# Performance work log

Measured on AMD Instinct MI355X. Metric: run time of the kernel, lower is better.

## Reference

```python
import jax, jax.numpy as jnp
import numpy as np


def _layernorm(x, g, b, eps=1e-5):
    m = x.mean(-1, keepdims=True)
    v = ((x - m) ** 2).mean(-1, keepdims=True)
    return (x - m) / jnp.sqrt(v + eps) * g + b


def _rotate_every_two(x):
    x1 = x[..., ::2]
    x2 = x[..., 1::2]
    return jnp.stack([-x2, x1], axis=-1).reshape(x.shape)


def _segsum(x):
    # x: (..., L) of negative decay rates -> (..., L, L) bidirectional segment sums
    cs = jnp.cumsum(x, axis=-1)
    d = cs[..., :, None] - cs[..., None, :]
    L = x.shape[-1]
    i = jnp.arange(L)[:, None]
    j = jnp.arange(L)[None, :]
    # lower-tri (incl diag): cs[i]-cs[j]; strict upper: cs[j]-cs[i]; diag is 0
    return jnp.where(i >= j, d, -d)


def _forward(x, y, th, dw1_w, dw1_b, dw2_w, dw2_b, qw, qb, kw, kb, vw, vb,
             lepe_w, lepe_b, dt_w, dt_bias, A_log, ow, ob,
             n1_g, n1_b, ffn_w1, ffn_b1, ffn_w2, ffn_b2, n2_g, n2_b):
    B, C, H, W = x.shape
    nh = dt_bias.shape[0]
    hd = C // nh
    scaling = hd ** (-0.5)

    # dynamic gated fusion of the two kv branches (1x1 convs == channel matmuls)
    fusion = jnp.concatenate([y, th], axis=1)                      # (B,2C,H,W)
    hid = jax.nn.relu(jnp.einsum('bchw,oc->bohw', fusion, dw1_w) + dw1_b[None, :, None, None])
    logits = jnp.einsum('bchw,oc->bohw', hid, dw2_w) + dw2_b[None, :, None, None]
    wts = jax.nn.softmax(logits, axis=1)                           # (B,2,H,W)
    fused = y * wts[:, 0:1] + th * wts[:, 1:2]

    xh = jnp.transpose(x, (0, 2, 3, 1))                            # (B,H,W,C)
    fkv = jnp.transpose(fused, (0, 2, 3, 1))

    # 2D RoPE tables (flattened raster index)
    angle = jnp.repeat(1.0 / 10000 ** jnp.linspace(0.0, 1.0, hd // 2), 2)
    idx = jnp.arange(H * W, dtype=x.dtype)
    sin = jnp.sin(idx[:, None] * angle[None, :]).reshape(H, W, hd)
    cos = jnp.cos(idx[:, None] * angle[None, :]).reshape(H, W, hd)

    q = xh @ qw + qb
    k = fkv @ kw + kb
    v = fkv @ vw + vb

    # depthwise 5x5 conv position term on v (NHWC)
    lepe = jax.lax.conv_general_dilated(
        v, lepe_w, (1, 1), ((2, 2), (2, 2)),
        dimension_numbers=('NHWC', 'HWIO', 'NHWC'), feature_group_count=C) + lepe_b

    k = k * scaling
    q = q.reshape(B, H, W, nh, hd).transpose(0, 3, 1, 2, 4)        # (B,nh,H,W,hd)
    k = k.reshape(B, H, W, nh, hd).transpose(0, 3, 1, 2, 4)
    v5 = v.reshape(B, H, W, nh, hd).transpose(0, 3, 1, 2, 4)

    qr = q * cos + _rotate_every_two(q) * sin
    kr = k * cos + _rotate_every_two(k) * sin

    # PathEmbeding2D: data-dependent decay masks
    xt = xh.reshape(B, H * W, nh, hd)
    dt = xt @ dt_w                                                 # (B,S,nh,2)
    A = -jnp.exp(A_log)                                            # (nh,)
    da = jax.nn.softplus(dt[..., 0] + dt_bias) * A                 # (B,S,nh)
    db = jax.nn.softplus(dt[..., 1] + dt_bias) * A
    mask_w = _segsum(da.reshape(B, H, W, nh).transpose(0, 1, 3, 2))  # (B,H,nh,W,W)
    mask_h = _segsum(db.reshape(B, H, W, nh).transpose(0, 2, 3, 1))  # (B,W,nh,H,H)

    # row (width-direction) and column (height-direction) attentions
    qk_w = jax.nn.softmax(jnp.einsum('bnhid,bnhjd->bhnij', qr, kr) + mask_w, axis=-1)  # (B,H,nh,W,W)
    qk_h = jax.nn.softmax(jnp.einsum('bnhwd,bngwd->bwnhg', qr, kr) + mask_h, axis=-1)  # (B,W,nh,H,H)

    v_w = jnp.einsum('bhnij,bnhjd->bhnid', qk_w, v5)               # (B,H,nh,W,hd)
    out1 = jnp.einsum('bwnhg,bgnwd->bwnhd', qk_h, v_w)             # (B,W,nh,H,hd)
    out1 = out1.transpose(0, 3, 1, 2, 4).reshape(B, H, W, C)

    v_h = jnp.einsum('bwnhg,bngwd->bwnhd', qk_h, v5)               # (B,W,nh,H,hd)
    out2 = jnp.einsum('bhnij,bjnhd->bhnid', qk_w, v_h)             # (B,H,nh,W,hd)
    out2 = out2.transpose(0, 1, 3, 2, 4).reshape(B, H, W, C)

    out = 0.5 * out1 + 0.5 * out2 + lepe
    out = out @ ow + ob
    out = _layernorm(xh + out, n1_g, n1_b)
    ffn = jax.nn.gelu(out @ ffn_w1 + ffn_b1, approximate=False) @ ffn_w2 + ffn_b2
    out = _layernorm(out + ffn, n2_g, n2_b)
    return jnp.transpose(out, (0, 3, 1, 2))                        # (B,C,H,W)


def setup_inputs() -> dict:
    B, C, H, W, nh = 4, 64, 128, 128, 4
    hd = C // nh
    key = jax.random.key(0)
    ks = jax.random.split(key, 20)
    n = lambda k, shp, s: jax.random.normal(k, shp, dtype=jnp.float32) * s
    rng = np.random.default_rng(0)
    dt = np.exp(rng.uniform(0.0, 1.0, nh) * (np.log(0.1) - np.log(0.001)) + np.log(0.001))
    dt = np.clip(dt, 1e-4, None)
    dt_bias = jnp.asarray(dt + np.log(-np.expm1(-dt)), dtype=jnp.float32)
    A_log = jnp.asarray(np.log(rng.uniform(1.0, 1.1, nh)), dtype=jnp.float32)
    inp = {
        'x': n(ks[0], (B, C, H, W), 1.0),
        'y': n(ks[1], (B, C, H, W), 1.0),
        'th': n(ks[2], (B, C, H, W), 1.0),
        'dw1_w': n(ks[3], (C, 2 * C), (2 * C) ** -0.5),
        'dw1_b': jnp.zeros((C,), jnp.float32),
        'dw2_w': n(ks[4], (2, C), C ** -0.5),
        'dw2_b': jnp.zeros((2,), jnp.float32),
        'qw': n(ks[5], (C, C), 0.2 * C ** -0.5),
        'qb': jnp.zeros((C,), jnp.float32),
        'kw': n(ks[6], (C, C), 0.2 * C ** -0.5),
        'kb': jnp.zeros((C,), jnp.float32),
        'vw': n(ks[7], (C, C), 0.2 * C ** -0.5),
        'vb': jnp.zeros((C,), jnp.float32),
        'lepe_w': n(ks[8], (5, 5, 1, C), 0.1),
        'lepe_b': jnp.zeros((C,), jnp.float32),
        'dt_w': n(ks[9], (hd, 2), hd ** -0.5),
        'dt_bias': dt_bias,
        'A_log': A_log,
        'ow': n(ks[10], (C, C), C ** -0.5),
        'ob': jnp.zeros((C,), jnp.float32),
        'n1_g': jnp.ones((C,), jnp.float32),
        'n1_b': jnp.zeros((C,), jnp.float32),
        'ffn_w1': n(ks[11], (C, 4 * C), C ** -0.5),
        'ffn_b1': jnp.zeros((4 * C,), jnp.float32),
        'ffn_w2': n(ks[12], (4 * C, C), (4 * C) ** -0.5),
        'ffn_b2': jnp.zeros((C,), jnp.float32),
        'n2_g': jnp.ones((C,), jnp.float32),
        'n2_b': jnp.zeros((C,), jnp.float32),
    }
    return inp


def reference(x, y, th, dw1_w, dw1_b, dw2_w, dw2_b, qw, qb, kw, kb, vw, vb,
              lepe_w, lepe_b, dt_w, dt_bias, A_log, ow, ob,
              n1_g, n1_b, ffn_w1, ffn_b1, ffn_w2, ffn_b2, n2_g, n2_b):
    return _forward(x, y, th, dw1_w, dw1_b, dw2_w, dw2_b, qw, qb, kw, kb, vw, vb,
                    lepe_w, lepe_b, dt_w, dt_bias, A_log, ow, ob,
                    n1_g, n1_b, ffn_w1, ffn_b1, ffn_w2, ffn_b2, n2_g, n2_b)
```

## Files before the change

kernel.cpp:

```cpp
#include <hip/hip_runtime.h>
#include <math.h>

#define HWSZ 16384

typedef __attribute__((ext_vector_type(8))) short bf16x8;
typedef __attribute__((ext_vector_type(4))) float f32x4;
typedef unsigned short u16;

union U4 { uint4 v; u16 s[8]; };
union U2 { uint2 v; u16 s[4]; };

__device__ __forceinline__ float gelu_f(float v) {
    return 0.5f * v * (1.0f + erff(v * 0.70710678118654752f));
}
__device__ __forceinline__ float splus_f(float v) {
    return (v > 20.f) ? v : log1pf(expf(v));
}
__device__ __forceinline__ u16 f2bf(float f) {
    union { float f; unsigned u; } v; v.f = f;
    unsigned r = (v.u + 0x7FFF + ((v.u >> 16) & 1)) >> 16;
    return (u16)r;
}
__device__ __forceinline__ unsigned pk2(float a, float b) {
    return (unsigned)f2bf(a) | ((unsigned)f2bf(b) << 16);
}
__device__ __forceinline__ float bf2f(u16 s) {
    union { unsigned u; float f; } v; v.u = ((unsigned)s) << 16; return v.f;
}

#define FS 136
__global__ __launch_bounds__(256) void k_fuse(
    const float* __restrict__ y, const float* __restrict__ th,
    const float* __restrict__ w1, const float* __restrict__ b1,
    const float* __restrict__ w2, const float* __restrict__ b2,
    u16* __restrict__ fused)
{
    __shared__ u16 Fsh[128*FS];
    __shared__ u16 Wt[64*FS];
    int tid = threadIdx.x, bid = blockIdx.x;
    int pbase = bid*128;
    int b = pbase >> 14, p0 = pbase & 16383;
    for (int vi = tid; vi < 1024; vi += 256) {
        int cp = vi >> 5;
        int p4 = (vi & 31)*4;
        int c0 = cp*2;
        float4 a = *(const float4*)&y [((size_t)(b*64+c0  ))*HWSZ + p0 + p4];
        float4 c = *(const float4*)&y [((size_t)(b*64+c0+1))*HWSZ + p0 + p4];
        *(unsigned*)&Fsh[(p4+0)*FS + c0] = pk2(a.x, c.x);
        *(unsigned*)&Fsh[(p4+1)*FS + c0] = pk2(a.y, c.y);
        *(unsigned*)&Fsh[(p4+2)*FS + c0] = pk2(a.z, c.z);
        *(unsigned*)&Fsh[(p4+3)*FS + c0] = pk2(a.w, c.w);
        float4 e = *(const float4*)&th[((size_t)(b*64+c0  ))*HWSZ + p0 + p4];
        float4 f = *(const float4*)&th[((size_t)(b*64+c0+1))*HWSZ + p0 + p4];
        *(unsigned*)&Fsh[(p4+0)*FS + 64 + c0] = pk2(e.x, f.x);
        *(unsigned*)&Fsh[(p4+1)*FS + 64 + c0] = pk2(e.y, f.y);
        *(unsigned*)&Fsh[(p4+2)*FS + 64 + c0] = pk2(e.z, f.z);
        *(unsigned*)&Fsh[(p4+3)*FS + 64 + c0] = pk2(e.w, f.w);
    }
    for (int vi = tid; vi < 2048; vi += 256) {
        int o = vi >> 5, c4 = (vi & 31)*4;
        float4 wv = *(const float4*)&w1[o*128 + c4];
        *(unsigned*)&Wt[o*FS + c4]     = pk2(wv.x, wv.y);
        *(unsigned*)&Wt[o*FS + c4 + 2] = pk2(wv.z, wv.w);
    }
    __syncthreads();
    int lane = tid & 63, wv = tid >> 6;
    int quad = lane >> 4, lm = lane & 15;
    int M0 = wv*32;
    f32x4 z = {0.f,0.f,0.f,0.f};
    f32x4 acc[2][4];
    #pragma unroll
    for (int mt = 0; mt < 2; ++mt)
        #pragma unroll
        for (int nt = 0; nt < 4; ++nt) acc[mt][nt] = z;
    #pragma unroll
    for (int ks = 0; ks < 4; ++ks) {
        bf16x8 aF[2];
        #pragma unroll
        for (int mt = 0; mt < 2; ++mt)
            aF[mt] = *(bf16x8*)&Fsh[(M0+mt*16+lm)*FS + ks*32 + quad*8];
        #pragma unroll
        for (int nt = 0; nt < 4; ++nt) {
            bf16x8 bW = *(bf16x8*)&Wt[(nt*16+lm)*FS + ks*32 + quad*8];
            #pragma unroll
            for (int mt = 0; mt < 2; ++mt)
                acc[mt][nt] = __builtin_amdgcn_mfma_f32_16x16x32_bf16(aF[mt], bW, acc[mt][nt], 0,0,0);
        }
    }
    float b1v[4], w2av[4], w2bv[4];
    #pragma unroll
    for (int nt = 0; nt < 4; ++nt) {
        int o = nt*16 + lm;
        b1v[nt] = b1[o]; w2av[nt] = w2[o]; w2bv[nt] = w2[64+o];
    }
    float bias2a = b2[0], bias2b = b2[1];
    size_t gbase = (size_t)(b*16384 + p0);
// ... 2 lines not shown
        #pragma unroll
        for (int r = 0; r < 4; ++r) {
            int p = M0 + mt*16 + quad*4 + r;
            float l0 = 0.f, l1 = 0.f;
            #pragma unroll
            for (int nt = 0; nt < 4; ++nt) {
                float h = fmaxf(acc[mt][nt][r] + b1v[nt], 0.f);
                l0 += h * w2av[nt];
                l1 += h * w2bv[nt];
            }
            l0 += __shfl_xor(l0,1,64); l0 += __shfl_xor(l0,2,64);
            l0 += __shfl_xor(l0,4,64); l0 += __shfl_xor(l0,8,64);
            l1 += __shfl_xor(l1,1,64); l1 += __shfl_xor(l1,2,64);
            l1 += __shfl_xor(l1,4,64); l1 += __shfl_xor(l1,8,64);
            l0 += bias2a; l1 += bias2b;
            float m = fmaxf(l0, l1);
            float e0 = __expf(l0 - m), e1 = __expf(l1 - m);
            float inv = 1.f/(e0 + e1);
            float wa = e0*inv, wb = e1*inv;
            U2 yv, tv;
            yv.v = *(uint2*)&Fsh[p*FS + lm*4];
            tv.v = *(uint2*)&Fsh[p*FS + 64 + lm*4];
            unsigned o0 = pk2(bf2f(yv.s[0])*wa + bf2f(tv.s[0])*wb,
                              bf2f(yv.s[1])*wa + bf2f(tv.s[1])*wb);
            unsigned o1 = pk2(bf2f(yv.s[2])*wa + bf2f(tv.s[2])*wb,
                              bf2f(yv.s[3])*wa + bf2f(tv.s[3])*wb);
            *(uint2*)&fused[(gbase + p)*64 + lm*4] = make_uint2(o0, o1);
        }
    }
}

__global__ __launch_bounds__(256) void k_qkv(
    const float* __restrict__ x, const u16* __restrict__ fused,
    const float* __restrict__ qw, const float* __restrict__ qb,
    const float* __restrict__ kw, const float* __restrict__ kb,
    const float* __restrict__ vw, const float* __restrict__ vb,
    const float* __restrict__ dtw, const float* __restrict__ dtb,
    const float* __restrict__ alog,
    u16* __restrict__ qr, u16* __restrict__ kr, u16* __restrict__ v5,
    float* __restrict__ da, float* __restrict__ db)
{
    __shared__ u16 Ax[128*72];
    __shared__ u16 Af[128*72];
    __shared__ u16 Bq[64*72], Bk[64*72], Bv[64*72];
    int tid = threadIdx.x, bid = blockIdx.x;
    int pbase = bid*128;
    int b = pbase >> 14, p0 = pbase & 16383;
    for (int vi = tid; vi < 2048; vi += 256) {
        int c = vi >> 5, pg = (vi & 31)*4;
        float4 xv = *(const float4*)&x[((size_t)(b*64+c))*HWSZ + p0 + pg];
        Ax[(pg+0)*72 + c] = f2bf(xv.x);
        Ax[(pg+1)*72 + c] = f2bf(xv.y);
        Ax[(pg+2)*72 + c] = f2bf(xv.z);
        Ax[(pg+3)*72 + c] = f2bf(xv.w);
    }
    for (int vi = tid; vi < 1024; vi += 256) {
        int p = vi >> 3, seg = (vi & 7)*8;
        *(uint4*)&Af[p*72 + seg] = *(const uint4*)&fused[((size_t)(b*16384) + p0 + p)*64 + seg];
    }
    for (int vi = tid; vi < 1024; vi += 256) {
        int c = vi >> 4, o4 = (vi & 15)*4;
        float4 q = *(const float4*)&qw[c*64 + o4];
        float4 k = *(const float4*)&kw[c*64 + o4];
        float4 v = *(const float4*)&vw[c*64 + o4];
        Bq[(o4+0)*72+c]=f2bf(q.x); Bq[(o4+1)*72+c]=f2bf(q.y); Bq[(o4+2)*72+c]=f2bf(q.z); Bq[(o4+3)*72+c]=f2bf(q.w);
        Bk[(o4+0)*72+c]=f2bf(k.x); Bk[(o4+1)*72+c]=f2bf(k.y); Bk[(o4+2)*72+c]=f2bf(k.z); Bk[(o4+3)*72+c]=f2bf(k.w);
        Bv[(o4+0)*72+c]=f2bf(v.x); Bv[(o4+1)*72+c]=f2bf(v.y); Bv[(o4+2)*72+c]=f2bf(v.z); Bv[(o4+3)*72+c]=f2bf(v.w);
    }
    __syncthreads();
    int lane = tid & 63, wv = tid >> 6;
    int quad = lane >> 4, lm = lane & 15;
    int M0 = wv*32;
    f32x4 z = {0.f,0.f,0.f,0.f};
    f32x4 accQ[2][4], accK[2][4], accV[2][4];
    #pragma unroll
    for (int mt = 0; mt < 2; ++mt)
        #pragma unroll
        for (int nt = 0; nt < 4; ++nt) { accQ[mt][nt]=z; accK[mt][nt]=z; accV[mt][nt]=z; }
    #pragma unroll
    for (int ks = 0; ks < 2; ++ks) {
        bf16x8 aX[2], aF[2];
        #pragma unroll
        for (int mt = 0; mt < 2; ++mt) {
            aX[mt] = *(bf16x8*)&Ax[(M0+mt*16+lm)*72 + ks*32 + quad*8];
            aF[mt] = *(bf16x8*)&Af[(M0+mt*16+lm)*72 + ks*32 + quad*8];
        }
        #pragma unroll
        for (int nt = 0; nt < 4; ++nt) {
            bf16x8 bQ = *(bf16x8*)&Bq[(nt*16+lm)*72 + ks*32 + quad*8];
            bf16x8 bK = *(bf16x8*)&Bk[(nt*16+lm)*72 + ks*32 + quad*8];
            bf16x8 bV = *(bf16x8*)&Bv[(nt*16+lm)*72 + ks*32 + quad*8];
            #pragma unroll
            for (int mt = 0; mt < 2; ++mt) {
                accQ[mt][nt] = __builtin_amdgcn_mfma_f32_16x16x32_bf16(aX[mt], bQ, accQ[mt][nt], 0,0,0);
                accK[mt][nt] = __builtin_amdgcn_mfma_f32_16x16x32_bf16(aF[mt], bK, accK[mt][nt], 0,0,0);
                accV[mt][nt] = __builtin_amdgcn_mfma_f32_16x16x32_bf16(aF[mt], bV, accV[mt][nt], 0,0,0);
            }
        }
    }
    {
        float dtw_[32];
        #pragma unroll
        for (int i = 0; i < 32; ++i) dtw_[i] = dtw[i];
        #pragma unroll
        for (int rep = 0; rep < 2; ++rep) {
            int pair = tid + rep*256;
            int p = pair >> 2, n = pair & 3;
            float dt0 = 0.f, dt1 = 0.f;
            #pragma unroll
            for (int d = 0; d < 16; ++d) {
                float xv = bf2f(Ax[p*72 + n*16 + d]);
                dt0 += xv*dtw_[2*d];
                dt1 += xv*dtw_[2*d+1];
            }
            float A = -expf(alog[n]);
            float bb = dtb[n];
            int P = p0 + p;
            int h = P >> 7, w = P & 127;
            da[((b*128+h)*4+n)*128 + w] = splus_f(dt0+bb)*A;
            db[((b*128+w)*4+n)*128 + h] = splus_f(dt1+bb)*A;
        }
    }
    float qbv[4], kbv[4], vbv[4];
    #pragma unroll
    for (int nt = 0; nt < 4; ++nt) {
        qbv[nt] = qb[nt*16+lm]; kbv[nt] = kb[nt*16+lm]; vbv[nt] = vb[nt*16+lm];
    }
    bool evn = !(lm & 1);
    float ang = exp2f(-1.89824462565f * (float)(lm >> 1));
    int bb4 = b*4;
    #pragma unroll
    for (int mt = 0; mt < 2; ++mt) {
        #pragma unroll
        for (int r = 0; r < 4; ++r) {
            int P = p0 + M0 + mt*16 + quad*4 + r;
            float sn_, cs_;
            sincosf((float)P * ang, &sn_, &cs_);
            #pragma unroll
            for (int nt = 0; nt < 4; ++nt) {
                float vq = accQ[mt][nt][r] + qbv[nt];
                float pq = __shfl_xor(vq, 1, 64);
                float rq = evn ? vq*cs_ - pq*sn_ : vq*cs_ + pq*sn_;
                unsigned uq = f2bf(rq);
                unsigned upq = (unsigned)__shfl_xor((int)uq, 1, 64);
                float vk = (accK[mt][nt][r] + kbv[nt])*0.25f;
                float pk = __shfl_xor(vk, 1, 64);
                float rk = evn ? vk*cs_ - pk*sn_ : vk*cs_ + pk*sn_;
                unsigned uk = f2bf(rk);
                unsigned upk = (unsigned)__shfl_xor((int)uk, 1, 64);
                unsigned uv = f2bf(accV[mt][nt][r] + vbv[nt]);
                unsigned upv = (unsigned)__shfl_xor((int)uv, 1, 64);
                if (evn) {
                    size_t off = ((size_t)(bb4+nt)*HWSZ + P)*16 + lm;
                    *(unsigned*)&qr[off] = (uq & 0xffff) | (upq << 16);
                    *(unsigned*)&kr[off] = (uk & 0xffff) | (upk << 16);
                    *(unsigned*)&v5[off] = (uv & 0xffff) | (upv << 16);
                }
            }
        }
    }
}

#define LROW 328
__global__ __launch_bounds__(256) void k_lepe(
    const u16* __restrict__ v5, const float* __restrict__ lw,
    const float* __restrict__ lb, u16* __restrict__ lepe)
{
    __shared__ float sv[36*LROW];
    __shared__ float swt[400];
    int tid = threadIdx.x, bid = blockIdx.x;
    int tw = bid & 7, th_ = (bid >> 3) & 3, n = (bid >> 5) & 3, b = bid >> 7;
    int bn = b*4 + n;
    int h0 = th_*32, w0 = tw*16;
    for (int i = tid; i < 400; i += 256) {
        int tap = i >> 4, d = i & 15;
        swt[i] = lw[tap*64 + n*16 + d];
    }
    const u16* vb = v5 + (size_t)bn*HWSZ*16;
// ... 349 lines not shown
    #pragma unroll
    for (int c = 0; c < 4; ++c) {
        bf16x8 bV  = *(bf16x8*)&Vt[lm*136 + c*32 + quad*8];
        bf16x8 aP0 = *(bf16x8*)&Ps[(r0+lm)*136 + c*32 + quad*8];
        bf16x8 aP1 = *(bf16x8*)&Ps[(r1+lm)*136 + c*32 + quad*8];
        acc0 = __builtin_amdgcn_mfma_f32_16x16x32_bf16(aP0, bV, acc0, 0,0,0);
        acc1 = __builtin_amdgcn_mfma_f32_16x16x32_bf16(aP1, bV, acc1, 0,0,0);
    }
    size_t lpb = (size_t)bn*262144 + (size_t)h*2048;
    size_t oab = (size_t)b*1048576 + (size_t)h*8192 + n*16;
    bool evn = !(lm & 1);
    #pragma unroll
    for (int r = 0; r < 4; ++r) {
        int i0 = r0+quad*4+r, i1 = r1+quad*4+r;
        float o2a = acc0[r]*linv[i0];
        float o2b = acc1[r]*linv[i1];
        float o1a = bf2f(o1b[vbase + (size_t)i0*2048 + lm]);
        float o1c = bf2f(o1b[vbase + (size_t)i1*2048 + lm]);
        float la  = bf2f(lepe[lpb + (size_t)i0*16 + lm]);
        float lc  = bf2f(lepe[lpb + (size_t)i1*16 + lm]);
        unsigned ua = f2bf(0.5f*(o1a + o2a) + la);
        unsigned uc = f2bf(0.5f*(o1c + o2b) + lc);
        unsigned upa = (unsigned)__shfl_xor((int)ua,1,64);
        unsigned upc = (unsigned)__shfl_xor((int)uc,1,64);
        if (evn) {
            *(unsigned*)&attn[oab + (size_t)i0*64 + lm] = (ua & 0xffff) | (upa << 16);
            *(unsigned*)&attn[oab + (size_t)i1*64 + lm] = (uc & 0xffff) | (upc << 16);
        }
    }
}

__global__ __launch_bounds__(256) void k_proj_ln(
    const u16* __restrict__ attn, const float* __restrict__ x,
    const float* __restrict__ ow, const float* __restrict__ ob,
    const float* __restrict__ g1, const float* __restrict__ b1,
    u16* __restrict__ t1)
{
    __shared__ u16 As[128*72];
    __shared__ u16 Bs[64*72];
    __shared__ float XT[8704];
    int tid = threadIdx.x, bid = blockIdx.x;
    int pbase = bid*128;
    int b = pbase >> 14, p0 = pbase & 16383;
    for (int vi = tid; vi < 1024; vi += 256) {
        int p = vi >> 3, seg = (vi & 7)*8;
        *(uint4*)&As[p*72 + seg] = *(const uint4*)&attn[((size_t)(pbase+p))*64 + seg];
    }
    for (int vi = tid; vi < 512; vi += 256) {
        int kp = vi >> 4, c4 = (vi & 15)*4;
        float4 a = *(const float4*)&ow[(2*kp)*64 + c4];
        float4 c = *(const float4*)&ow[(2*kp+1)*64 + c4];
        *(unsigned*)&Bs[(c4+0)*72 + 2*kp] = pk2(a.x, c.x);
        *(unsigned*)&Bs[(c4+1)*72 + 2*kp] = pk2(a.y, c.y);
        *(unsigned*)&Bs[(c4+2)*72 + 2*kp] = pk2(a.z, c.z);
        *(unsigned*)&Bs[(c4+3)*72 + 2*kp] = pk2(a.w, c.w);
    }
    for (int vi = tid; vi < 2048; vi += 256) {
        int c = vi >> 5, p4 = (vi & 31)*4;
        *(float4*)&XT[c*132 + p4] = *(const float4*)&x[((size_t)(b*64+c))*HWSZ + p0 + p4];
    }
    __syncthreads();
    int lane = tid & 63, wv = tid >> 6;
    int quad = lane >> 4, lm = lane & 15;
    int M0 = wv*32;
    float xv[2][4][4], obv[4], g1v[4], b1v[4];
    #pragma unroll
    for (int nt = 0; nt < 4; ++nt) {
        int c = nt*16 + lm;
        obv[nt] = ob[c]; g1v[nt] = g1[c]; b1v[nt] = b1[c];
        #pragma unroll
        for (int mt = 0; mt < 2; ++mt)
            #pragma unroll
            for (int r = 0; r < 4; ++r)
                xv[mt][nt][r] = XT[c*132 + M0 + mt*16 + quad*4 + r];
    }
    f32x4 z = {0.f,0.f,0.f,0.f};
    f32x4 acc[2][4];
    #pragma unroll
    for (int mt = 0; mt < 2; ++mt)
        #pragma unroll
        for (int nt = 0; nt < 4; ++nt) acc[mt][nt] = z;
    #pragma unroll
    for (int ks = 0; ks < 2; ++ks) {
        bf16x8 aF[2];
        #pragma unroll
        for (int mt = 0; mt < 2; ++mt)
            aF[mt] = *(bf16x8*)&As[(M0+mt*16+lm)*72 + ks*32 + quad*8];
        #pragma unroll
        for (int nt = 0; nt < 4; ++nt) {
            bf16x8 bF = *(bf16x8*)&Bs[(nt*16+lm)*72 + ks*32 + quad*8];
            #pragma unroll
            for (int mt = 0; mt < 2; ++mt)
                acc[mt][nt] = __builtin_amdgcn_mfma_f32_16x16x32_bf16(aF[mt], bF, acc[mt][nt], 0,0,0);
        }
    }
    float val[2][4][4], res[2][4][4];
    #pragma unroll
    for (int mt = 0; mt < 2; ++mt) {
        #pragma unroll
        for (int r = 0; r < 4; ++r) {
            float s = 0.f;
            #pragma unroll
            for (int nt = 0; nt < 4; ++nt) {
                val[mt][nt][r] = acc[mt][nt][r] + obv[nt] + xv[mt][nt][r];
                s += val[mt][nt][r];
            }
            s += __shfl_xor(s, 1, 64); s += __shfl_xor(s, 2, 64);
            s += __shfl_xor(s, 4, 64); s += __shfl_xor(s, 8, 64);
            float mean = s*(1.f/64.f);
            float vv = 0.f;
            #pragma unroll
            for (int nt = 0; nt < 4; ++nt) {
                float d = val[mt][nt][r] - mean;
                vv += d*d;
            }
            vv += __shfl_xor(vv, 1, 64); vv += __shfl_xor(vv, 2, 64);
            vv += __shfl_xor(vv, 4, 64); vv += __shfl_xor(vv, 8, 64);
            float rs = rsqrtf(vv*(1.f/64.f) + 1e-5f);
            #pragma unroll
            for (int nt = 0; nt < 4; ++nt)
                res[mt][nt][r] = (val[mt][nt][r] - mean)*rs*g1v[nt] + b1v[nt];
        }
    }
    __syncthreads();
    float* outT = XT;
    #pragma unroll
    for (int mt = 0; mt < 2; ++mt)
        #pragma unroll
        for (int r = 0; r < 4; ++r)
            #pragma unroll
            for (int nt = 0; nt < 4; ++nt)
                outT[(M0+mt*16+quad*4+r)*68 + nt*16 + lm] = res[mt][nt][r];
    __syncthreads();
    for (int vi = tid; vi < 1024; vi += 256) {
        int p = vi >> 3, seg = (vi & 7)*8;
        float4 f0 = *(const float4*)&outT[p*68 + seg];
        float4 f1 = *(const float4*)&outT[p*68 + seg + 4];
        uint4 o = make_uint4(pk2(f0.x,f0.y), pk2(f0.z,f0.w), pk2(f1.x,f1.y), pk2(f1.z,f1.w));
        *(uint4*)&t1[((size_t)(pbase+p))*64 + seg] = o;
    }
}

__global__ __launch_bounds__(256) void k_ffn(
    const u16* __restrict__ t1, const float* __restrict__ w1,
    const float* __restrict__ b1f, const float* __restrict__ w2,
    const float* __restrict__ b2f, const float* __restrict__ g2,
    const float* __restrict__ bb2, float* __restrict__ outp)
{
    __shared__ u16 At1[128*72];
    __shared__ u16 WH[2*64*72 + 128*72];
    __shared__ float sb1[256];
    __shared__ float sb2[64], sg[64], sbb[64];
    u16* W1b = WH;
    u16* W2b = WH + 4608;
    u16* Hid = WH + 9216;
    int tid = threadIdx.x, bid = blockIdx.x;
    int pbase = bid*128;
    int b = pbase >> 14, p0 = pbase & 16383;
    for (int vi = tid; vi < 1024; vi += 256) {
        int p = vi >> 3, seg = (vi & 7)*8;
        *(uint4*)&At1[p*72 + seg] = *(const uint4*)&t1[((size_t)(pbase+p))*64 + seg];
    }
    if (tid < 256) sb1[tid] = b1f[tid];
    if (tid < 64) { sb2[tid] = b2f[tid]; sg[tid] = g2[tid]; sbb[tid] = bb2[tid]; }
    int lane = tid & 63, wv = tid >> 6;
    int quad = lane >> 4, lm = lane & 15;
    int M0 = wv*32;
    f32x4 z = {0.f,0.f,0.f,0.f};
    f32x4 acc2[2][4];
    #pragma unroll
    for (int mt = 0; mt < 2; ++mt)
        #pragma unroll
        for (int nt = 0; nt < 4; ++nt) acc2[mt][nt] = z;
    for (int jc = 0; jc < 4; ++jc) {
        __syncthreads();
        for (int vi = tid; vi < 512; vi += 256) {
            int kp = vi >> 4, c4 = (vi & 15)*4;
            float4 a = *(const float4*)&w1[(2*kp)*256 + jc*64 + c4];
            float4 c = *(const float4*)&w1[(2*kp+1)*256 + jc*64 + c4];
            *(unsigned*)&W1b[(c4+0)*72 + 2*kp] = pk2(a.x, c.x);
            *(unsigned*)&W1b[(c4+1)*72 + 2*kp] = pk2(a.y, c.y);
            *(unsigned*)&W1b[(c4+2)*72 + 2*kp] = pk2(a.z, c.z);
            *(unsigned*)&W1b[(c4+3)*72 + 2*kp] = pk2(a.w, c.w);
        }
        for (int vi = tid; vi < 512; vi += 256) {
            int kp = vi >> 4, c4 = (vi & 15)*4;
            float4 a = *(const float4*)&w2[(size_t)(jc*64 + 2*kp)*64 + c4];
            float4 c = *(const float4*)&w2[(size_t)(jc*64 + 2*kp+1)*64 + c4];
            *(unsigned*)&W2b[(c4+0)*72 + 2*kp] = pk2(a.x, c.x);
            *(unsigned*)&W2b[(c4+1)*72 + 2*kp] = pk2(a.y, c.y);
            *(unsigned*)&W2b[(c4+2)*72 + 2*kp] = pk2(a.z, c.z);
            *(unsigned*)&W2b[(c4+3)*72 + 2*kp] = pk2(a.w, c.w);
        }
        __syncthreads();
        f32x4 h[2][4];
        #pragma unroll
        for (int mt = 0; mt < 2; ++mt)
            #pragma unroll
            for (int nt = 0; nt < 4; ++nt) h[mt][nt] = z;
        #pragma unroll
        for (int ks = 0; ks < 2; ++ks) {
            bf16x8 aF[2];
            #pragma unroll
            for (int mt = 0; mt < 2; ++mt)
                aF[mt] = *(bf16x8*)&At1[(M0+mt*16+lm)*72 + ks*32 + quad*8];
            #pragma unroll
            for (int nt = 0; nt < 4; ++nt) {
                bf16x8 bF = *(bf16x8*)&W1b[(nt*16+lm)*72 + ks*32 + quad*8];
                #pragma unroll
                for (int mt = 0; mt < 2; ++mt)
                    h[mt][nt] = __builtin_amdgcn_mfma_f32_16x16x32_bf16(aF[mt], bF, h[mt][nt], 0,0,0);
            }
        }
        #pragma unroll
        for (int nt = 0; nt < 4; ++nt) {
            float bb = sb1[jc*64 + nt*16 + lm];
            #pragma unroll
            for (int mt = 0; mt < 2; ++mt)
                #pragma unroll
                for (int r = 0; r < 4; ++r) {
                    float hv = gelu_f(h[mt][nt][r] + bb);
                    unsigned u = (unsigned)f2bf(hv);
                    unsigned up = (unsigned)__shfl_xor((int)u, 1, 64);
                    if (!(lm & 1))
                        *(unsigned*)&Hid[(M0+mt*16+quad*4+r)*72 + nt*16 + lm] = (u & 0xffff) | (up << 16);
                }
        }
        #pragma unroll
        for (int ks = 0; ks < 2; ++ks) {
            bf16x8 aH[2];
            #pragma unroll
            for (int mt = 0; mt < 2; ++mt)
                aH[mt] = *(bf16x8*)&Hid[(M0+mt*16+lm)*72 + ks*32 + quad*8];
            #pragma unroll
            for (int nt = 0; nt < 4; ++nt) {
                bf16x8 bF = *(bf16x8*)&W2b[(nt*16+lm)*72 + ks*32 + quad*8];
                #pragma unroll
                for (int mt = 0; mt < 2; ++mt)
                    acc2[mt][nt] = __builtin_amdgcn_mfma_f32_16x16x32_bf16(aH[mt], bF, acc2[mt][nt], 0,0,0);
            }
        }
    }
    float val[2][4][4], res[2][4][4];
    float sb2v[4], sgv[4], sbbv[4];
    #pragma unroll
    for (int nt = 0; nt < 4; ++nt) {
        int c = nt*16 + lm;
        sb2v[nt] = sb2[c]; sgv[nt] = sg[c]; sbbv[nt] = sbb[c];
    }
    #pragma unroll
    for (int mt = 0; mt < 2; ++mt) {
        #pragma unroll
        for (int r = 0; r < 4; ++r) {
            int pos = M0 + mt*16 + quad*4 + r;
            float s = 0.f;
            #pragma unroll
            for (int nt = 0; nt < 4; ++nt) {
                float tv = bf2f(At1[pos*72 + nt*16 + lm]);
                val[mt][nt][r] = acc2[mt][nt][r] + sb2v[nt] + tv;
                s += val[mt][nt][r];
            }
            s += __shfl_xor(s, 1, 64); s += __shfl_xor(s, 2, 64);
            s += __shfl_xor(s, 4, 64); s += __shfl_xor(s, 8, 64);
            float mean = s*(1.f/64.f);
            float vv = 0.f;
            #pragma unroll
            for (int nt = 0; nt < 4; ++nt) {
                float d = val[mt][nt][r] - mean;
                vv += d*d;
            }
            vv += __shfl_xor(vv, 1, 64); vv += __shfl_xor(vv, 2, 64);
            vv += __shfl_xor(vv, 4, 64); vv += __shfl_xor(vv, 8, 64);
            float rs = rsqrtf(vv*(1.f/64.f) + 1e-5f);
            #pragma unroll
            for (int nt = 0; nt < 4; ++nt)
                res[mt][nt][r] = (val[mt][nt][r] - mean)*rs*sgv[nt] + sbbv[nt];
        }
    }
    __syncthreads();
    float* outT = (float*)WH;
    #pragma unroll
    for (int mt = 0; mt < 2; ++mt)
        #pragma unroll
        for (int r = 0; r < 4; ++r)
            #pragma unroll
            for (int nt = 0; nt < 4; ++nt)
                outT[(nt*16+lm)*132 + M0 + mt*16 + quad*4 + r] = res[mt][nt][r];
    __syncthreads();
    for (int vi = tid; vi < 2048; vi += 256) {
        int c = vi >> 5, p4 = (vi & 31)*4;
        *(float4*)&outp[((size_t)(b*64+c))*HWSZ + p0 + p4] = *(const float4*)&outT[c*132 + p4];
    }
}

extern "C" void kernel_launch(void* const* d_in, const int* in_sizes, int n_in,
                              void* d_out, int out_size, void* d_ws, size_t ws_size,
                              hipStream_t stream) {
    const float* x      = (const float*)d_in[0];
    const float* y      = (const float*)d_in[1];
    const float* th     = (const float*)d_in[2];
    const float* dw1_w  = (const float*)d_in[3];
    const float* dw1_b  = (const float*)d_in[4];
    const float* dw2_w  = (const float*)d_in[5];
    const float* dw2_b  = (const float*)d_in[6];
    const float* qw     = (const float*)d_in[7];
    const float* qb     = (const float*)d_in[8];
    const float* kw     = (const float*)d_in[9];
    const float* kb     = (const float*)d_in[10];
    const float* vw     = (const float*)d_in[11];
    const float* vb     = (const float*)d_in[12];
    const float* lepe_w = (const float*)d_in[13];
    const float* lepe_b = (const float*)d_in[14];
    const float* dt_w   = (const float*)d_in[15];
    const float* dt_bias= (const float*)d_in[16];
    const float* A_log  = (const float*)d_in[17];
    const float* ow     = (const float*)d_in[18];
    const float* ob     = (const float*)d_in[19];
    const float* n1_g   = (const float*)d_in[20];
    const float* n1_b   = (const float*)d_in[21];
    const float* ffn_w1 = (const float*)d_in[22];
    const float* ffn_b1 = (const float*)d_in[23];
    const float* ffn_w2 = (const float*)d_in[24];
    const float* ffn_b2 = (const float*)d_in[25];
    const float* n2_g   = (const float*)d_in[26];
    const float* n2_b   = (const float*)d_in[27];
    float* out = (float*)d_out;

    const size_t SZ = 4194304;
    float* ws    = (float*)d_ws;
    u16* fused = (u16*)(ws + 0*SZ);
    u16* qrb   = (u16*)(ws + 1*SZ);
    u16* krb   = (u16*)(ws + 2*SZ);
    u16* v5b   = (u16*)(ws + 3*SZ);
    u16* lepeb = (u16*)(ws + 4*SZ);
    u16* vhb   = (u16*)(ws + 5*SZ);
    u16* o1b   = (u16*)(ws + 6*SZ);
    u16* attnb = (u16*)(ws + 7*SZ);
    u16* t1b   = (u16*)(ws + 8*SZ);
    float* dacs  = ws + 9*SZ;
    float* dbcs  = ws + 9*SZ + 262144;

    k_fuse<<<512, 256, 0, stream>>>(y, th, dw1_w, dw1_b, dw2_w, dw2_b, fused);
    k_qkv<<<512, 256, 0, stream>>>(x, fused, qw, qb, kw, kb, vw, vb,
                                   dt_w, dt_bias, A_log, qrb, krb, v5b, dacs, dbcs);
    k_lepe<<<512, 256, 0, stream>>>(v5b, lepe_w, lepe_b, lepeb);
    k_attn_w1<<<2048, 256, 0, stream>>>(qrb, krb, v5b, dacs, fused);
    k_attn_h<<<2048, 256, 0, stream>>>(qrb, krb, v5b, fused, dbcs, vhb, o1b);
    k_attn_w2<<<2048, 256, 0, stream>>>(qrb, krb, vhb, o1b, dacs, lepeb, attnb);
    k_proj_ln<<<512, 256, 0, stream>>>(attnb, x, ow, ob, n1_g, n1_b, t1b);
    k_ffn<<<512, 256, 0, stream>>>(t1b, ffn_w1, ffn_b1, ffn_w2, ffn_b2, n2_g, n2_b, out);
}
```

Baseline: 314.4 us.

## Pre-convert weights to bf16 once and halve row tiles in proj/FFN kernels

```diff
diff --git a/kernel.cpp b/kernel.cpp
--- a/kernel.cpp
+++ b/kernel.cpp
@@ -28,10 +28,40 @@
     union { unsigned u; float f; } v; v.u = ((unsigned)s) << 16; return v.f;
 }
 
+__global__ __launch_bounds__(256) void k_prep(
+    const float* __restrict__ w1, const float* __restrict__ qw,
+    const float* __restrict__ kw, const float* __restrict__ vw,
+    const float* __restrict__ ow, const float* __restrict__ fw1s,
+    const float* __restrict__ fw2s, u16* __restrict__ wout)
+{
+    int id = blockIdx.x*256 + threadIdx.x;
+    float v;
+    if (id < 8192) {
+        v = w1[id];
+    } else if (id < 20480) {
+        int t = id - 8192; int m = t >> 12;
+        int i = t & 4095; int o = i >> 6, c = i & 63;
+        const float* src = (m==0) ? qw : ((m==1) ? kw : vw);
+        v = src[c*64 + o];
+        if (m == 1) v *= 0.25f;
+    } else if (id < 24576) {
+        int i = id - 20480; int c = i >> 6, k = i & 63;
+        v = ow[k*64 + c];
+    } else if (id < 40960) {
+        int i = id - 24576; int o = i >> 6, k = i & 63;
+        v = fw1s[k*256 + o];
+    } else {
+        int i = id - 40960; int jc = i >> 12; int r = i & 4095;
+        int c = r >> 6, k2 = r & 63;
+        v = fw2s[(jc*64 + k2)*64 + c];
+    }
+    wout[id] = f2bf(v);
+}
+
 #define FS 136
 __global__ __launch_bounds__(256) void k_fuse(
     const float* __restrict__ y, const float* __restrict__ th,
-    const float* __restrict__ w1, const float* __restrict__ b1,
+    const u16* __restrict__ wfuse, const float* __restrict__ b1,
     const float* __restrict__ w2, const float* __restrict__ b2,
     u16* __restrict__ fused)
 {
@@ -57,11 +87,9 @@
         *(unsigned*)&Fsh[(p4+2)*FS + 64 + c0] = pk2(e.z, f.z);
         *(unsigned*)&Fsh[(p4+3)*FS + 64 + c0] = pk2(e.w, f.w);
     }
-    for (int vi = tid; vi < 2048; vi += 256) {
-        int o = vi >> 5, c4 = (vi & 31)*4;
-        float4 wv = *(const float4*)&w1[o*128 + c4];
-        *(unsigned*)&Wt[o*FS + c4]     = pk2(wv.x, wv.y);
-        *(unsigned*)&Wt[o*FS + c4 + 2] = pk2(wv.z, wv.w);
+    for (int vi = tid; vi < 1024; vi += 256) {
+        int o = vi >> 4, s8 = (vi & 15)*8;
+        *(uint4*)&Wt[o*FS + s8] = *(const uint4*)&wfuse[o*128 + s8];
     }
     __syncthreads();
     int lane = tid & 63, wv = tid >> 6;
@@ -130,9 +158,9 @@
 
 __global__ __launch_bounds__(256) void k_qkv(
     const float* __restrict__ x, const u16* __restrict__ fused,
-    const float* __restrict__ qw, const float* __restrict__ qb,
-    const float* __restrict__ kw, const float* __restrict__ kb,
-    const float* __restrict__ vw, const float* __restrict__ vb,
+    const u16* __restrict__ bq, const float* __restrict__ qb,
+    const u16* __restrict__ bk, const float* __restrict__ kb,
+    const u16* __restrict__ bv, const float* __restrict__ vb,
     const float* __restrict__ dtw, const float* __restrict__ dtb,
     const float* __restrict__ alog,
     u16* __restrict__ qr, u16* __restrict__ kr, u16* __restrict__ v5,
@@ -156,14 +184,13 @@
         int p = vi >> 3, seg = (vi & 7)*8;
         *(uint4*)&Af[p*72 + seg] = *(const uint4*)&fused[((size_t)(b*16384) + p0 + p)*64 + seg];
     }
-    for (int vi = tid; vi < 1024; vi += 256) {
-        int c = vi >> 4, o4 = (vi & 15)*4;
-        float4 q = *(const float4*)&qw[c*64 + o4];
-        float4 k = *(const float4*)&kw[c*64 + o4];
-        float4 v = *(const float4*)&vw[c*64 + o4];
-        Bq[(o4+0)*72+c]=f2bf(q.x); Bq[(o4+1)*72+c]=f2bf(q.y); Bq[(o4+2)*72+c]=f2bf(q.z); Bq[(o4+3)*72+c]=f2bf(q.w);
-        Bk[(o4+0)*72+c]=f2bf(k.x); Bk[(o4+1)*72+c]=f2bf(k.y); Bk[(o4+2)*72+c]=f2bf(k.z); Bk[(o4+3)*72+c]=f2bf(k.w);
-        Bv[(o4+0)*72+c]=f2bf(v.x); Bv[(o4+1)*72+c]=f2bf(v.y); Bv[(o4+2)*72+c]=f2bf(v.z); Bv[(o4+3)*72+c]=f2bf(v.w);
+    for (int vi = tid; vi < 1536; vi += 256) {
+        int m = vi >> 9;
+        int i = vi & 511;
+        int o = i >> 3, s8 = (i & 7)*8;
+        const u16* src = (m==0) ? bq : ((m==1) ? bk : bv);
+        u16* dst = (m==0) ? Bq : ((m==1) ? Bk : Bv);
+        *(uint4*)&dst[o*72 + s8] = *(const uint4*)&src[o*64 + s8];
     }
     __syncthreads();
     int lane = tid & 63, wv = tid >> 6;
@@ -222,7 +249,7 @@
     float qbv[4], kbv[4], vbv[4];
     #pragma unroll
     for (int nt = 0; nt < 4; ++nt) {
-        qbv[nt] = qb[nt*16+lm]; kbv[nt] = kb[nt*16+lm]; vbv[nt] = vb[nt*16+lm];
+        qbv[nt] = qb[nt*16+lm]; kbv[nt] = kb[nt*16+lm]*0.25f; vbv[nt] = vb[nt*16+lm];
     }
     bool evn = !(lm & 1);
     float ang = exp2f(-1.89824462565f * (float)(lm >> 1));
@@ -241,7 +268,7 @@
                 float rq = evn ? vq*cs_ - pq*sn_ : vq*cs_ + pq*sn_;
                 unsigned uq = f2bf(rq);
                 unsigned upq = (unsigned)__shfl_xor((int)uq, 1, 64);
-                float vk = (accK[mt][nt][r] + kbv[nt])*0.25f;
+                float vk = accK[mt][nt][r] + kbv[nt];
                 float pk = __shfl_xor(vk, 1, 64);
                 float rk = evn ? vk*cs_ - pk*sn_ : vk*cs_ + pk*sn_;
                 unsigned uk = f2bf(rk);
@@ -657,216 +684,169 @@
 
 __global__ __launch_bounds__(256) void k_proj_ln(
     const u16* __restrict__ attn, const float* __restrict__ x,
-    const float* __restrict__ ow, const float* __restrict__ ob,
+    const u16* __restrict__ bo, const float* __restrict__ ob,
     const float* __restrict__ g1, const float* __restrict__ b1,
     u16* __restrict__ t1)
 {
-    __shared__ u16 As[128*72];
+    __shared__ u16 As[64*72];
     __shared__ u16 Bs[64*72];
-    __shared__ float XT[8704];
+    __shared__ float XT[64*68];
     int tid = threadIdx.x, bid = blockIdx.x;
-    int pbase = bid*128;
+    int pbase = bid*64;
     int b = pbase >> 14, p0 = pbase & 16383;
+    for (int vi = tid; vi < 512; vi += 256) {
+        int p = vi >> 3, s8 = (vi & 7)*8;
+        *(uint4*)&As[p*72 + s8] = *(const uint4*)&attn[((size_t)(pbase+p))*64 + s8];
+    }
+    for (int vi = tid; vi < 512; vi += 256) {
+        int c = vi >> 3, s8 = (vi & 7)*8;
+        *(uint4*)&Bs[c*72 + s8] = *(const uint4*)&bo[c*64 + s8];
+    }
     for (int vi = tid; vi < 1024; vi += 256) {
-        int p = vi >> 3, seg = (vi & 7)*8;
-        *(uint4*)&As[p*72 + seg] = *(const uint4*)&attn[((size_t)(pbase+p))*64 + seg];
-    }
-    for (int vi = tid; vi < 512; vi += 256) {
-        int kp = vi >> 4, c4 = (vi & 15)*4;
-        float4 a = *(const float4*)&ow[(2*kp)*64 + c4];
-        float4 c = *(const float4*)&ow[(2*kp+1)*64 + c4];
-        *(unsigned*)&Bs[(c4+0)*72 + 2*kp] = pk2(a.x, c.x);
-        *(unsigned*)&Bs[(c4+1)*72 + 2*kp] = pk2(a.y, c.y);
-        *(unsigned*)&Bs[(c4+2)*72 + 2*kp] = pk2(a.z, c.z);
-        *(unsigned*)&Bs[(c4+3)*72 + 2*kp] = pk2(a.w, c.w);
-    }
-    for (int vi = tid; vi < 2048; vi += 256) {
-        int c = vi >> 5, p4 = (vi & 31)*4;
-        *(float4*)&XT[c*132 + p4] = *(const float4*)&x[((size_t)(b*64+c))*HWSZ + p0 + p4];
+        int c = vi >> 4, p4 = (vi & 15)*4;
+        *(float4*)&XT[c*68 + p4] = *(const float4*)&x[((size_t)(b*64+c))*HWSZ + p0 + p4];
     }
     __syncthreads();
     int lane = tid & 63, wv = tid >> 6;
     int quad = lane >> 4, lm = lane & 15;
-    int M0 = wv*32;
-    float xv[2][4][4], obv[4], g1v[4], b1v[4];
+    int M0 = wv*16;
+    float xv[4][4], obv[4], g1v[4], b1v[4];
     #pragma unroll
     for (int nt = 0; nt < 4; ++nt) {
         int c = nt*16 + lm;
         obv[nt] = ob[c]; g1v[nt] = g1[c]; b1v[nt] = b1[c];
         #pragma unroll
-        for (int mt = 0; mt < 2; ++mt)
-            #pragma unroll
-            for (int r = 0; r < 4; ++r)
-                xv[mt][nt][r] = XT[c*132 + M0 + mt*16 + quad*4 + r];
+        for (int r = 0; r < 4; ++r)
+            xv[nt][r] = XT[c*68 + M0 + quad*4 + r];
     }
     f32x4 z = {0.f,0.f,0.f,0.f};
-    f32x4 acc[2][4];
-    #pragma unroll
-    for (int mt = 0; mt < 2; ++mt)
-        #pragma unroll
-        for (int nt = 0; nt < 4; ++nt) acc[mt][nt] = z;
+    f32x4 acc[4];
+    #pragma unroll
+    for (int nt = 0; nt < 4; ++nt) acc[nt] = z;
     #pragma unroll
     for (int ks = 0; ks < 2; ++ks) {
-        bf16x8 aF[2];
-        #pragma unroll
-        for (int mt = 0; mt < 2; ++mt)
-            aF[mt] = *(bf16x8*)&As[(M0+mt*16+lm)*72 + ks*32 + quad*8];
+        bf16x8 aF = *(bf16x8*)&As[(M0+lm)*72 + ks*32 + quad*8];
         #pragma unroll
         for (int nt = 0; nt < 4; ++nt) {
             bf16x8 bF = *(bf16x8*)&Bs[(nt*16+lm)*72 + ks*32 + quad*8];
-            #pragma unroll
-            for (int mt = 0; mt < 2; ++mt)
-                acc[mt][nt] = __builtin_amdgcn_mfma_f32_16x16x32_bf16(aF[mt], bF, acc[mt][nt], 0,0,0);
-        }
-    }
-    float val[2][4][4], res[2][4][4];
-    #pragma unroll
-    for (int mt = 0; mt < 2; ++mt) {
-        #pragma unroll
-        for (int r = 0; r < 4; ++r) {
-            float s = 0.f;
-            #pragma unroll
-            for (int nt = 0; nt < 4; ++nt) {
-                val[mt][nt][r] = acc[mt][nt][r] + obv[nt] + xv[mt][nt][r];
-                s += val[mt][nt][r];
-            }
-            s += __shfl_xor(s, 1, 64); s += __shfl_xor(s, 2, 64);
-            s += __shfl_xor(s, 4, 64); s += __shfl_xor(s, 8, 64);
-            float mean = s*(1.f/64.f);
-            float vv = 0.f;
-            #pragma unroll
-            for (int nt = 0; nt < 4; ++nt) {
-                float d = val[mt][nt][r] - mean;
-                vv += d*d;
-            }
-            vv += __shfl_xor(vv, 1, 64); vv += __shfl_xor(vv, 2, 64);
-            vv += __shfl_xor(vv, 4, 64); vv += __shfl_xor(vv, 8, 64);
-            float rs = rsqrtf(vv*(1.f/64.f) + 1e-5f);
-            #pragma unroll
-            for (int nt = 0; nt < 4; ++nt)
-                res[mt][nt][r] = (val[mt][nt][r] - mean)*rs*g1v[nt] + b1v[nt];
-        }
+            acc[nt] = __builtin_amdgcn_mfma_f32_16x16x32_bf16(aF, bF, acc[nt], 0,0,0);
+        }
+    }
+    float val[4][4], res[4][4];
+    #pragma unroll
+    for (int r = 0; r < 4; ++r) {
+        float s = 0.f;
+        #pragma unroll
+        for (int nt = 0; nt < 4; ++nt) {
+            val[nt][r] = acc[nt][r] + obv[nt] + xv[nt][r];
+            s += val[nt][r];
+        }
+        s += __shfl_xor(s, 1, 64); s += __shfl_xor(s, 2, 64);
+        s += __shfl_xor(s, 4, 64); s += __shfl_xor(s, 8, 64);
+        float mean = s*(1.f/64.f);
+        float vv = 0.f;
+        #pragma unroll
+        for (int nt = 0; nt < 4; ++nt) {
+            float d = val[nt][r] - mean;
+            vv += d*d;
+        }
+        vv += __shfl_xor(vv, 1, 64); vv += __shfl_xor(vv, 2, 64);
+        vv += __shfl_xor(vv, 4, 64); vv += __shfl_xor(vv, 8, 64);
+        float rs = rsqrtf(vv*(1.f/64.f) + 1e-5f);
+        #pragma unroll
+        for (int nt = 0; nt < 4; ++nt)
+            res[nt][r] = (val[nt][r] - mean)*rs*g1v[nt] + b1v[nt];
     }
     __syncthreads();
     float* outT = XT;
     #pragma unroll
-    for (int mt = 0; mt < 2; ++mt)
-        #pragma unroll
-        for (int r = 0; r < 4; ++r)
-            #pragma unroll
-            for (int nt = 0; nt < 4; ++nt)
-                outT[(M0+mt*16+quad*4+r)*68 + nt*16 + lm] = res[mt][nt][r];
-    __syncthreads();
-    for (int vi = tid; vi < 1024; vi += 256) {
-        int p = vi >> 3, seg = (vi & 7)*8;
-        float4 f0 = *(const float4*)&outT[p*68 + seg];
-        float4 f1 = *(const float4*)&outT[p*68 + seg + 4];
+    for (int r = 0; r < 4; ++r)
+        #pragma unroll
+        for (int nt = 0; nt < 4; ++nt)
+            outT[(M0+quad*4+r)*68 + nt*16 + lm] = res[nt][r];
+    __syncthreads();
+    for (int vi = tid; vi < 512; vi += 256) {
+        int p = vi >> 3, s8 = (vi & 7)*8;
+        float4 f0 = *(const float4*)&outT[p*68 + s8];
+        float4 f1 = *(const float4*)&outT[p*68 + s8 + 4];
         uint4 o = make_uint4(pk2(f0.x,f0.y), pk2(f0.z,f0.w), pk2(f1.x,f1.y), pk2(f1.z,f1.w));
-        *(uint4*)&t1[((size_t)(pbase+p))*64 + seg] = o;
+        *(uint4*)&t1[((size_t)(pbase+p))*64 + s8] = o;
     }
 }
 
 __global__ __launch_bounds__(256) void k_ffn(
-    const u16* __restrict__ t1, const float* __restrict__ w1,
-    const float* __restrict__ b1f, const float* __restrict__ w2,
+    const u16* __restrict__ t1, const u16* __restrict__ fw1,
+    const float* __restrict__ b1f, const u16* __restrict__ fw2,
     const float* __restrict__ b2f, const float* __restrict__ g2,
     const float* __restrict__ bb2, float* __restrict__ outp)
 {
-    __shared__ u16 At1[128*72];
-    __shared__ u16 WH[2*64*72 + 128*72];
+    __shared__ u16 SL[18432];
     __shared__ float sb1[256];
     __shared__ float sb2[64], sg[64], sbb[64];
-    u16* W1b = WH;
-    u16* W2b = WH + 4608;
-    u16* Hid = WH + 9216;
+    u16* At1 = SL;
+    u16* W1b = SL + 4608;
+    u16* W2b = SL + 9216;
+    u16* Hid = SL + 13824;
     int tid = threadIdx.x, bid = blockIdx.x;
-    int pbase = bid*128;
+    int pbase = bid*64;
     int b = pbase >> 14, p0 = pbase & 16383;
-    for (int vi = tid; vi < 1024; vi += 256) {
-        int p = vi >> 3, seg = (vi & 7)*8;
-        *(uint4*)&At1[p*72 + seg] = *(const uint4*)&t1[((size_t)(pbase+p))*64 + seg];
+    for (int vi = tid; vi < 512; vi += 256) {
+        int p = vi >> 3, s8 = (vi & 7)*8;
+        *(uint4*)&At1[p*72 + s8] = *(const uint4*)&t1[((size_t)(pbase+p))*64 + s8];
     }
     if (tid < 256) sb1[tid] = b1f[tid];
     if (tid < 64) { sb2[tid] = b2f[tid]; sg[tid] = g2[tid]; sbb[tid] = bb2[tid]; }
     int lane = tid & 63, wv = tid >> 6;
     int quad = lane >> 4, lm = lane & 15;
-    int M0 = wv*32;
+    int M0 = wv*16;
     f32x4 z = {0.f,0.f,0.f,0.f};
-    f32x4 acc2[2][4];
-    #pragma unroll
-    for (int mt = 0; mt < 2; ++mt)
-        #pragma unroll
-        for (int nt = 0; nt < 4; ++nt) acc2[mt][nt] = z;
+    f32x4 acc2[4];
+    #pragma unroll
+    for (int nt = 0; nt < 4; ++nt) acc2[nt] = z;
     for (int jc = 0; jc < 4; ++jc) {
         __syncthreads();
-        for (int vi = tid; vi < 512; vi += 256) {
-            int kp = vi >> 4, c4 = (vi & 15)*4;
-            float4 a = *(const float4*)&w1[(2*kp)*256 + jc*64 + c4];
-            float4 c = *(const float4*)&w1[(2*kp+1)*256 + jc*64 + c4];
-            *(unsigned*)&W1b[(c4+0)*72 + 2*kp] = pk2(a.x, c.x);
-            *(unsigned*)&W1b[(c4+1)*72 + 2*kp] = pk2(a.y, c.y);
-            *(unsigned*)&W1b[(c4+2)*72 + 2*kp] = pk2(a.z, c.z);
-            *(unsigned*)&W1b[(c4+3)*72 + 2*kp] = pk2(a.w, c.w);
-        }
-        for (int vi = tid; vi < 512; vi += 256) {
-            int kp = vi >> 4, c4 = (vi & 15)*4;
-            float4 a = *(const float4*)&w2[(size_t)(jc*64 + 2*kp)*64 + c4];
-            float4 c = *(const float4*)&w2[(size_t)(jc*64 + 2*kp+1)*64 + c4];
-            *(unsigned*)&W2b[(c4+0)*72 + 2*kp] = pk2(a.x, c.x);
-            *(unsigned*)&W2b[(c4+1)*72 + 2*kp] = pk2(a.y, c.y);
-            *(unsigned*)&W2b[(c4+2)*72 + 2*kp] = pk2(a.z, c.z);
-            *(unsigned*)&W2b[(c4+3)*72 + 2*kp] = pk2(a.w, c.w);
+        for (int vi = tid; vi < 1024; vi += 256) {
+            int m = vi >> 9, i = vi & 511;
+            int o = i >> 3, s8 = (i & 7)*8;
+            if (m == 0) *(uint4*)&W1b[o*72 + s8] = *(const uint4*)&fw1[(jc*64+o)*64 + s8];
+            else        *(uint4*)&W2b[o*72 + s8] = *(const uint4*)&fw2[jc*4096 + o*64 + s8];
         }
         __syncthreads();
-        f32x4 h[2][4];
-        #pragma unroll
-        for (int mt = 0; mt < 2; ++mt)
-            #pragma unroll
-            for (int nt = 0; nt < 4; ++nt) h[mt][nt] = z;
+        f32x4 h[4];
+        #pragma unroll
+        for (int nt = 0; nt < 4; ++nt) h[nt] = z;
         #pragma unroll
         for (int ks = 0; ks < 2; ++ks) {
-            bf16x8 aF[2];
-            #pragma unroll
-            for (int mt = 0; mt < 2; ++mt)
-                aF[mt] = *(bf16x8*)&At1[(M0+mt*16+lm)*72 + ks*32 + quad*8];
+            bf16x8 aF = *(bf16x8*)&At1[(M0+lm)*72 + ks*32 + quad*8];
             #pragma unroll
             for (int nt = 0; nt < 4; ++nt) {
                 bf16x8 bF = *(bf16x8*)&W1b[(nt*16+lm)*72 + ks*32 + quad*8];
-                #pragma unroll
-                for (int mt = 0; mt < 2; ++mt)
-                    h[mt][nt] = __builtin_amdgcn_mfma_f32_16x16x32_bf16(aF[mt], bF, h[mt][nt], 0,0,0);
+                h[nt] = __builtin_amdgcn_mfma_f32_16x16x32_bf16(aF, bF, h[nt], 0,0,0);
             }
         }
         #pragma unroll
         for (int nt = 0; nt < 4; ++nt) {
             float bb = sb1[jc*64 + nt*16 + lm];
             #pragma unroll
-            for (int mt = 0; mt < 2; ++mt)
-                #pragma unroll
-                for (int r = 0; r < 4; ++r) {
-                    float hv = gelu_f(h[mt][nt][r] + bb);
-                    unsigned u = (unsigned)f2bf(hv);
-                    unsigned up = (unsigned)__shfl_xor((int)u, 1, 64);
-                    if (!(lm & 1))
-                        *(unsigned*)&Hid[(M0+mt*16+quad*4+r)*72 + nt*16 + lm] = (u & 0xffff) | (up << 16);
-                }
+            for (int r = 0; r < 4; ++r) {
+                float hv = gelu_f(h[nt][r] + bb);
+                unsigned u = (unsigned)f2bf(hv);
+                unsigned up = (unsigned)__shfl_xor((int)u, 1, 64);
+                if (!(lm & 1))
+                    *(unsigned*)&Hid[(M0+quad*4+r)*72 + nt*16 + lm] = (u & 0xffff) | (up << 16);
+            }
         }
         #pragma unroll
         for (int ks = 0; ks < 2; ++ks) {
-            bf16x8 aH[2];
-            #pragma unroll
-            for (int mt = 0; mt < 2; ++mt)
-                aH[mt] = *(bf16x8*)&Hid[(M0+mt*16+lm)*72 + ks*32 + quad*8];
+            bf16x8 aH = *(bf16x8*)&Hid[(M0+lm)*72 + ks*32 + quad*8];
             #pragma unroll
             for (int nt = 0; nt < 4; ++nt) {
                 bf16x8 bF = *(bf16x8*)&W2b[(nt*16+lm)*72 + ks*32 + quad*8];
-                #pragma unroll
-                for (int mt = 0; mt < 2; ++mt)
-                    acc2[mt][nt] = __builtin_amdgcn_mfma_f32_16x16x32_bf16(aH[mt], bF, acc2[mt][nt], 0,0,0);
+                acc2[nt] = __builtin_amdgcn_mfma_f32_16x16x32_bf16(aH, bF, acc2[nt], 0,0,0);
             }
         }
     }
-    float val[2][4][4], res[2][4][4];
+    float val[4][4], res[4][4];
     float sb2v[4], sgv[4], sbbv[4];
     #pragma unroll
     for (int nt = 0; nt < 4; ++nt) {
@@ -874,47 +854,42 @@
         sb2v[nt] = sb2[c]; sgv[nt] = sg[c]; sbbv[nt] = sbb[c];
     }
     #pragma unroll
-    for (int mt = 0; mt < 2; ++mt) {
-        #pragma unroll
-        for (int r = 0; r < 4; ++r) {
-            int pos = M0 + mt*16 + quad*4 + r;
-            float s = 0.f;
-            #pragma unroll
-            for (int nt = 0; nt < 4; ++nt) {
-                float tv = bf2f(At1[pos*72 + nt*16 + lm]);
-                val[mt][nt][r] = acc2[mt][nt][r] + sb2v[nt] + tv;
-                s += val[mt][nt][r];
-            }
-            s += __shfl_xor(s, 1, 64); s += __shfl_xor(s, 2, 64);
-            s += __shfl_xor(s, 4, 64); s += __shfl_xor(s, 8, 64);
-            float mean = s*(1.f/64.f);
-            float vv = 0.f;
-            #pragma unroll
-            for (int nt = 0; nt < 4; ++nt) {
-                float d = val[mt][nt][r] - mean;
-                vv += d*d;
-            }
-            vv += __shfl_xor(vv, 1, 64); vv += __shfl_xor(vv, 2, 64);
-            vv += __shfl_xor(vv, 4, 64); vv += __shfl_xor(vv, 8, 64);
-            float rs = rsqrtf(vv*(1.f/64.f) + 1e-5f);
-            #pragma unroll
-            for (int nt = 0; nt < 4; ++nt)
-                res[mt][nt][r] = (val[mt][nt][r] - mean)*rs*sgv[nt] + sbbv[nt];
-        }
-    }
-    __syncthreads();
-    float* outT = (float*)WH;
-    #pragma unroll
-    for (int mt = 0; mt < 2; ++mt)
-        #pragma unroll
-        for (int r = 0; r < 4; ++r)
-            #pragma unroll
-            for (int nt = 0; nt < 4; ++nt)
-                outT[(nt*16+lm)*132 + M0 + mt*16 + quad*4 + r] = res[mt][nt][r];
-    __syncthreads();
-    for (int vi = tid; vi < 2048; vi += 256) {
-        int c = vi >> 5, p4 = (vi & 31)*4;
-        *(float4*)&outp[((size_t)(b*64+c))*HWSZ + p0 + p4] = *(const float4*)&outT[c*132 + p4];
+    for (int r = 0; r < 4; ++r) {
+        int pos = M0 + quad*4 + r;
+        float s = 0.f;
+        #pragma unroll
+        for (int nt = 0; nt < 4; ++nt) {
+            float tv = bf2f(At1[pos*72 + nt*16 + lm]);
+            val[nt][r] = acc2[nt][r] + sb2v[nt] + tv;
+            s += val[nt][r];
+        }
+        s += __shfl_xor(s, 1, 64); s += __shfl_xor(s, 2, 64);
+        s += __shfl_xor(s, 4, 64); s += __shfl_xor(s, 8, 64);
+        float mean = s*(1.f/64.f);
+        float vv = 0.f;
+        #pragma unroll
+        for (int nt = 0; nt < 4; ++nt) {
+            float d = val[nt][r] - mean;
+            vv += d*d;
+        }
+        vv += __shfl_xor(vv, 1, 64); vv += __shfl_xor(vv, 2, 64);
+        vv += __shfl_xor(vv, 4, 64); vv += __shfl_xor(vv, 8, 64);
+        float rs = rsqrtf(vv*(1.f/64.f) + 1e-5f);
+        #pragma unroll
+        for (int nt = 0; nt < 4; ++nt)
+            res[nt][r] = (val[nt][r] - mean)*rs*sgv[nt] + sbbv[nt];
+    }
+    __syncthreads();
+    float* outT = (float*)SL;
+    #pragma unroll
+    for (int r = 0; r < 4; ++r)
+        #pragma unroll
+        for (int nt = 0; nt < 4; ++nt)
+            outT[(nt*16+lm)*68 + M0 + quad*4 + r] = res[nt][r];
+    __syncthreads();
+    for (int vi = tid; vi < 1024; vi += 256) {
+        int c = vi >> 4, p4 = (vi & 15)*4;
+        *(float4*)&outp[((size_t)(b*64+c))*HWSZ + p0 + p4] = *(const float4*)&outT[c*68 + p4];
     }
 }
 
@@ -964,14 +939,23 @@
     u16* t1b   = (u16*)(ws + 8*SZ);
     float* dacs  = ws + 9*SZ;
     float* dbcs  = ws + 9*SZ + 262144;
-
-    k_fuse<<<512, 256, 0, stream>>>(y, th, dw1_w, dw1_b, dw2_w, dw2_b, fused);
-    k_qkv<<<512, 256, 0, stream>>>(x, fused, qw, qb, kw, kb, vw, vb,
+    u16* wall  = (u16*)(ws + 9*SZ + 524288);
+    u16* wfuse = wall;
+    u16* bq    = wall + 8192;
+    u16* bk    = wall + 12288;
+    u16* bv    = wall + 16384;
+    u16* bo    = wall + 20480;
+    u16* fw1   = wall + 24576;
+    u16* fw2   = wall + 40960;
+
+    k_prep<<<224, 256, 0, stream>>>(dw1_w, qw, kw, vw, ow, ffn_w1, ffn_w2, wall);
+    k_fuse<<<512, 256, 0, stream>>>(y, th, wfuse, dw1_b, dw2_w, dw2_b, fused);
+    k_qkv<<<512, 256, 0, stream>>>(x, fused, bq, qb, bk, kb, bv, vb,
                                    dt_w, dt_bias, A_log, qrb, krb, v5b, dacs, dbcs);
     k_lepe<<<512, 256, 0, stream>>>(v5b, lepe_w, lepe_b, lepeb);
     k_attn_w1<<<2048, 256, 0, stream>>>(qrb, krb, v5b, dacs, fused);
     k_attn_h<<<2048, 256, 0, stream>>>(qrb, krb, v5b, fused, dbcs, vhb, o1b);
     k_attn_w2<<<2048, 256, 0, stream>>>(qrb, krb, vhb, o1b, dacs, lepeb, attnb);
-    k_proj_ln<<<512, 256, 0, stream>>>(attnb, x, ow, ob, n1_g, n1_b, t1b);
-    k_ffn<<<512, 256, 0, stream>>>(t1b, ffn_w1, ffn_b1, ffn_w2, ffn_b2, n2_g, n2_b, out);
-}
+    k_proj_ln<<<1024, 256, 0, stream>>>(attnb, x, bo, ob, n1_g, n1_b, t1b);
+    k_ffn<<<1024, 256, 0, stream>>>(t1b, fw1, ffn_b1, fw2, ffn_b2, n2_g, n2_b, out);
+}
```

Measured after the change: 304.0 us. 3.3% less time.
